# Kernel tuning notes

Measured on AMD Instinct MI355X. Metric: run time of the kernel, lower is better.

## Reference

```python
import jax, jax.numpy as jnp
import numpy as np

N_USER, N_VIDEO, N_PUB, N_TAG = 200000, 100000, 20000, 5000
EMB = 128
HALF = EMB // 2
LAYER_NUM = 3


def setup_inputs() -> dict:
    key = jax.random.key(0)
    ks = jax.random.split(key, 20)
    inp = {
        "user_emb": jax.random.normal(ks[0], (N_USER, EMB), jnp.float32),
        "video_emb": jax.random.normal(ks[1], (N_VIDEO, EMB), jnp.float32),
        "publisher_emb": jax.random.normal(ks[2], (N_PUB, EMB), jnp.float32),
        "tag_emb": jax.random.normal(ks[3], (N_TAG, EMB), jnp.float32),
    }
    # (name, E, n_src, n_dst)
    rels = [
        ("uv", 1500000, N_USER, N_VIDEO),
        ("vu", 1500000, N_VIDEO, N_USER),
        ("up", 800000, N_USER, N_PUB),
        ("pu", 800000, N_PUB, N_USER),
        ("vt", 800000, N_VIDEO, N_TAG),
        ("tv", 800000, N_TAG, N_VIDEO),
        ("pt", 400000, N_PUB, N_TAG),
        ("tp", 400000, N_TAG, N_PUB),
    ]
    for i, (name, E, ns, nd) in enumerate(rels):
        inp[name + "_src"] = jax.random.randint(ks[4 + 2 * i], (E,), 0, ns, jnp.int32)
        inp[name + "_dst"] = jax.random.randint(ks[5 + 2 * i], (E,), 0, nd, jnp.int32)
    return inp


def _seg_mean(feat, src, dst, num_dst):
    # copy_u + mean: gather half-dim src features, segment-mean onto dst.
    msg = feat[src]                                             # [E, HALF]
    s = jax.ops.segment_sum(msg, dst, num_segments=num_dst)     # [num_dst, HALF]
    deg = jax.ops.segment_sum(jnp.ones_like(dst, dtype=feat.dtype), dst,
                              num_segments=num_dst)
    return s / jnp.maximum(deg, 1.0)[:, None]  # zero-in-degree nodes -> 0 (DGL behavior)


def reference(user_emb, video_emb, publisher_emb, tag_emb,
              uv_src, uv_dst, vu_src, vu_dst,
              up_src, up_dst, pu_src, pu_dst,
              vt_src, vt_dst, tv_src, tv_dst,
              pt_src, pt_dst, tp_src, tp_dst):

    def layer(u, v, p, t):
        # user dst: [vu, pu]; video dst: [uv, tv]; publisher dst: [up, tp]; tag dst: [vt, pt]
        vu = _seg_mean(v[:, :HALF], vu_src, vu_dst, N_USER)
        pu = _seg_mean(p[:, :HALF], pu_src, pu_dst, N_USER)
        uv = _seg_mean(u[:, :HALF], uv_src, uv_dst, N_VIDEO)
        tv = _seg_mean(t[:, :HALF], tv_src, tv_dst, N_VIDEO)
        up = _seg_mean(u[:, HALF:], up_src, up_dst, N_PUB)
        tp = _seg_mean(t[:, HALF:], tp_src, tp_dst, N_PUB)
        vt = _seg_mean(v[:, HALF:], vt_src, vt_dst, N_TAG)
        pt = _seg_mean(p[:, HALF:], pt_src, pt_dst, N_TAG)
        return (jnp.concatenate([vu, pu], axis=1),
                jnp.concatenate([uv, tv], axis=1),
                jnp.concatenate([up, tp], axis=1),
                jnp.concatenate([vt, pt], axis=1))

    pu_, pv_, pp_, pt_ = user_emb, video_emb, publisher_emb, tag_emb
    u, v, p, t = user_emb, video_emb, publisher_emb, tag_emb
    for i in range(LAYER_NUM):
        u, v, p, t = layer(u, v, p, t)
        w = 1.0 / (i + 2)
        pu_ = pu_ + u * w
        pv_ = pv_ + v * w
        pp_ = pp_ + p * w
        pt_ = pt_ + t * w
    return (pu_, pv_, pp_, pt_)
```

## Files before the change

kernel.cpp:

```cpp
#include <hip/hip_runtime.h>
#include <hip/hip_bf16.h>
#include <stdint.h>

#define EMB 128
#define CAP 12288

static constexpr int N_USER = 200000, N_VIDEO = 100000, N_PUB = 20000, N_TAG = 5000;
static constexpr int ROW_U = 0, ROW_V = 200000, ROW_P = 300000, ROW_T = 320000;
static constexpr int ROWS = 325000;
static constexpr int TOTAL_E = 7000000;
static constexpr int TOTAL_GROUPS = 650000;
static constexpr int TILE = 4096;

__device__ inline unsigned bf16_rne(float f) {
  unsigned u = __float_as_uint(f);
  return (u + 0x7fffu + ((u >> 16) & 1u)) >> 16;
}
__device__ inline unsigned pack_bf16x2(float lo, float hi) {
  return bf16_rne(lo) | (bf16_rne(hi) << 16);
}

struct SortDesc {
  int tcum[9];
  int bcum[9];
  int gcum[8];
  int E[8];
  int n_dst[8];
  int wshift[8];
  const int* esrc[8];
  const int* edst[8];
};

struct AggrDesc {
  int cum[9];
  int src_base[8];
  int src_col[8];
  int dst_base[8];
  int dst_col[8];
  const float* demb[8];
};

__global__ __launch_bounds__(256) void part_kernel(SortDesc d, uint2* __restrict__ pairs,
                                                   int* __restrict__ cursors) {
  __shared__ int cnt[256];
  __shared__ int lcur[256];
  int blk = blockIdx.x;
  int r = 0;
#pragma unroll
  for (int k = 1; k < 8; ++k) if (blk >= d.tcum[k]) r = k;
  int base = (blk - d.tcum[r]) * TILE;
  int n = min(TILE, d.E[r] - base);
  const int* __restrict__ esrc = d.esrc[r];
  const int* __restrict__ edst = d.edst[r];
  int tid = threadIdx.x;
  int B = d.bcum[r + 1] - d.bcum[r];
  int sh = d.wshift[r];
  int bb = d.bcum[r];
  if (tid < B) cnt[tid] = 0;
  __syncthreads();
  for (int i = tid; i < n; i += 256)
    atomicAdd(&cnt[edst[base + i] >> sh], 1);
  __syncthreads();
  if (tid < B) {
    int c = cnt[tid];
    lcur[tid] = c ? atomicAdd(&cursors[bb + tid], c) : 0;
  }
  __syncthreads();
  for (int i = tid; i < n; i += 256) {
    int dv = edst[base + i];
    int sv = esrc[base + i];
    int b = dv >> sh;
    int pos = atomicAdd(&lcur[b], 1);
    if (pos < CAP) {
      uint2 pr; pr.x = (unsigned)sv; pr.y = (unsigned)dv;
      pairs[(size_t)(bb + b) * CAP + pos] = pr;
    }
  }
}

__global__ __launch_bounds__(256) void bases_kernel(const int* __restrict__ cursors,
                                                    int* __restrict__ bases, int NB) {
  __shared__ int wsums[4];
  int tid = threadIdx.x;
  int L = (NB + 255) / 256;
  int lo = min(tid * L, NB), hi = min(lo + L, NB);
  int s = 0;
  for (int i = lo; i < hi; ++i) s += cursors[i];
  int lane = tid & 63, wv = tid >> 6;
  int v = s;
#pragma unroll
  for (int dd = 1; dd < 64; dd <<= 1) {
    int t = __shfl_up(v, dd);
    if (lane >= dd) v += t;
  }
  if (lane == 63) wsums[wv] = v;
  __syncthreads();
  if (tid == 0) {
    int run = 0;
#pragma unroll
    for (int k = 0; k < 4; ++k) { int t = wsums[k]; wsums[k] = run; run += t; }
  }
  __syncthreads();
  int run = wsums[wv] + (v - s);
  for (int i = lo; i < hi; ++i) { int c = cursors[i]; bases[i] = run; run += c; }
}

__global__ __launch_bounds__(256) void build_kernel(SortDesc d, const uint2* __restrict__ pairs,
                                                    const int* __restrict__ cursors,
                                                    const int* __restrict__ bases,
                                                    int* __restrict__ sorted,
                                                    int* __restrict__ Beg, int* __restrict__ Deg) {
  __shared__ int cnt[1024];
  __shared__ int stage[CAP];
  __shared__ int wsums[4];
  int bucket = blockIdx.x;
  int r = 0;
#pragma unroll
  for (int k = 1; k < 8; ++k) if (bucket >= d.bcum[k]) r = k;
  int bl = bucket - d.bcum[r];
  int sh = d.wshift[r];
  int first = bl << sh;
  int Wa = min(1 << sh, d.n_dst[r] - first);
  int tid = threadIdx.x;
  int n_b = min(cursors[bucket], CAP);
  int gbase = bases[bucket];
  const uint2* __restrict__ bp = pairs + (size_t)bucket * CAP;

  for (int i = tid; i < 1024; i += 256) cnt[i] = 0;
  __syncthreads();
  for (int i = tid; i < n_b; i += 256)
    atomicAdd(&cnt[(int)bp[i].y - first], 1);
  __syncthreads();

  int t4 = tid * 4;
  int c0 = cnt[t4], c1 = cnt[t4 + 1], c2 = cnt[t4 + 2], c3 = cnt[t4 + 3];
  int s = c0 + c1 + c2 + c3;
  int lane = tid & 63, wv = tid >> 6;
  int v = s;
#pragma unroll
  for (int dd = 1; dd < 64; dd <<= 1) {
    int t = __shfl_up(v, dd);
    if (lane >= dd) v += t;
  }
  if (lane == 63) wsums[wv] = v;
  __syncthreads();
  if (tid == 0) {
    int run = 0;
#pragma unroll
    for (int k = 0; k < 4; ++k) { int t = wsums[k]; wsums[k] = run; run += t; }
  }
  __syncthreads();
  int ex = wsums[wv] + (v - s);
  int o0 = ex, o1 = ex + c0, o2 = o1 + c1, o3 = o2 + c2;
  cnt[t4] = o0; cnt[t4 + 1] = o1; cnt[t4 + 2] = o2; cnt[t4 + 3] = o3;
  int g0 = d.gcum[r] + first + t4;
  if (t4 + 0 < Wa) { Beg[g0 + 0] = gbase + o0; Deg[g0 + 0] = c0; }
  if (t4 + 1 < Wa) { Beg[g0 + 1] = gbase + o1; Deg[g0 + 1] = c1; }
  if (t4 + 2 < Wa) { Beg[g0 + 2] = gbase + o2; Deg[g0 + 2] = c2; }
  if (t4 + 3 < Wa) { Beg[g0 + 3] = gbase + o3; Deg[g0 + 3] = c3; }
  __syncthreads();

  for (int i = tid; i < n_b; i += 256) {
    uint2 pr = bp[i];
    int pos = atomicAdd(&cnt[(int)pr.y - first], 1);
    stage[pos] = (int)pr.x;
  }
  __syncthreads();
  for (int i = tid; i < n_b; i += 256)
    sorted[gbase + i] = stage[i];
}

__global__ void convert_kernel(const float* __restrict__ u, const float* __restrict__ v,
                               const float* __restrict__ p, const float* __restrict__ t,
                               uint16_t* __restrict__ feat) {
  int idx = blockIdx.x * blockDim.x + threadIdx.x;
  const int total4 = ROWS * EMB / 4;
  if (idx >= total4) return;
  int flat = idx * 4;
  int row = flat >> 7;
  int col = flat & 127;
  const float* s;
  if (row < ROW_V)      s = u + (size_t)row * EMB + col;
  else if (row < ROW_P) s = v + (size_t)(row - ROW_V) * EMB + col;
  else if (row < ROW_T) s = p + (size_t)(row - ROW_P) * EMB + col;
  else                  s = t + (size_t)(row - ROW_T) * EMB + col;
  float4 f = *(const float4*)s;
  uint2 o;
  o.x = pack_bf16x2(f.x, f.y);
  o.y = pack_bf16x2(f.z, f.w);
  *(uint2*)(feat + flat) = o;
}

#define ACC(q) \
  a0 += __uint_as_float((q).x << 16); a1 += __uint_as_float((q).x & 0xffff0000u); \
  a2 += __uint_as_float((q).y << 16); a3 += __uint_as_float((q).y & 0xffff0000u); \
  a4 += __uint_as_float((q).z << 16); a5 += __uint_as_float((q).z & 0xffff0000u); \
  a6 += __uint_as_float((q).w << 16); a7 += __uint_as_float((q).w & 0xffff0000u);

__global__ __launch_bounds__(256) void aggr_kernel(AggrDesc d, const uint16_t* __restrict__ prev,
                                                   uint16_t* __restrict__ next,
                                                   float* __restrict__ out, float w,
                                                   int layer0, int writeNext,
                                                   const int* __restrict__ sorted,
                                                   const int* __restrict__ Beg,
                                                   const int* __restrict__ Deg) {
  int g = blockIdx.x * 32 + (threadIdx.x >> 3);
  if (g >= TOTAL_GROUPS) return;
  int lane = threadIdx.x & 7;
  int r = 0;
#pragma unroll
  for (int k = 1; k < 8; ++k) if (g >= d.cum[k]) r = k;
  int n = g - d.cum[r];
  int beg = Beg[g], dg = Deg[g];
  float recip = 1.0f / (float)(dg > 0 ? dg : 1);
  const uint16_t* sbase = prev + (size_t)d.src_base[r] * EMB + d.src_col[r] + lane * 8;
  float a0 = 0.f, a1 = 0.f, a2 = 0.f, a3 = 0.f, a4 = 0.f, a5 = 0.f, a6 = 0.f, a7 = 0.f;
  int e = beg, end = beg + dg;
  for (; e + 4 <= end; e += 4) {
    int s0 = sorted[e], s1 = sorted[e + 1], s2 = sorted[e + 2], s3 = sorted[e + 3];
    uint4 q0 = *(const uint4*)(sbase + (size_t)s0 * EMB);
    uint4 q1 = *(const uint4*)(sbase + (size_t)s1 * EMB);
    uint4 q2 = *(const uint4*)(sbase + (size_t)s2 * EMB);
    uint4 q3 = *(const uint4*)(sbase + (size_t)s3 * EMB);
    ACC(q0); ACC(q1); ACC(q2); ACC(q3);
  }
  for (; e < end; ++e) {
    int s0 = sorted[e];
    uint4 q = *(const uint4*)(sbase + (size_t)s0 * EMB);
    ACC(q);
  }
  a0 *= recip; a1 *= recip; a2 *= recip; a3 *= recip;
  a4 *= recip; a5 *= recip; a6 *= recip; a7 *= recip;

  int col = d.dst_col[r] + lane * 8;
  size_t dpos = (size_t)(d.dst_base[r] + n) * EMB + col;
  if (writeNext) {
    uint4 ov;
    ov.x = pack_bf16x2(a0, a1);
    ov.y = pack_bf16x2(a2, a3);
    ov.z = pack_bf16x2(a4, a5);
    ov.w = pack_bf16x2(a6, a7);
    *(uint4*)(next + dpos) = ov;
  }
  float4 v0, v1;
  if (layer0) {
    const float* de = d.demb[r] + (size_t)n * EMB + col;
    v0 = *(const float4*)de;
    v1 = *((const float4*)de + 1);
  } else {
    v0 = *(const float4*)(out + dpos);
    v1 = *((const float4*)(out + dpos) + 1);
  }
  v0.x += w * a0; v0.y += w * a1; v0.z += w * a2; v0.w += w * a3;
  v1.x += w * a4; v1.y += w * a5; v1.z += w * a6; v1.w += w * a7;
  *(float4*)(out + dpos) = v0;
  *((float4*)(out + dpos) + 1) = v1;
}

extern "C" void kernel_launch(void* const* d_in, const int* in_sizes, int n_in,
                              void* d_out, int out_size, void* d_ws, size_t ws_size,
                              hipStream_t stream) {
  const float* emb_u = (const float*)d_in[0];
  const float* emb_v = (const float*)d_in[1];
  const float* emb_p = (const float*)d_in[2];
  const float* emb_t = (const float*)d_in[3];

  struct RelInfo { int si, di, E, n_dst, src_base, src_col, dst_base, dst_col, wshift; };
  const RelInfo rels[8] = {
    {12, 13,  800000, N_TAG,   ROW_V, 64, ROW_T,  0,  5},
    {16, 17,  400000, N_TAG,   ROW_P, 64, ROW_T, 64,  5},
    { 8,  9,  800000, N_PUB,   ROW_U, 64, ROW_P,  0,  7},
    {18, 19,  400000, N_PUB,   ROW_T, 64, ROW_P, 64,  7},
    { 4,  5, 1500000, N_VIDEO, ROW_U,  0, ROW_V,  0,  9},
    {14, 15,  800000, N_VIDEO, ROW_T,  0, ROW_V, 64,  9},
    { 6,  7, 1500000, N_USER,  ROW_V,  0, ROW_U,  0, 10},
    {10, 11,  800000, N_PUB ,  ROW_P,  0, ROW_U, 64, 10},
  };
  const float* dembs[8] = {emb_t, emb_t, emb_p, emb_p, emb_v, emb_v, emb_u, emb_u};

  char* ws = (char*)d_ws;
  size_t cursor = 0;
  auto take = [&](size_t bytes) -> char* {
    char* p = ws + cursor;
    cursor = (cursor + bytes + 255) & ~(size_t)255;
    return p;
  };
  uint16_t* featA = (uint16_t*)take((size_t)ROWS * EMB * 2);
  uint16_t* featB = (uint16_t*)take((size_t)ROWS * EMB * 2);
  int* sorted = (int*)take((size_t)TOTAL_E * 4);
  int* Beg    = (int*)take((size_t)TOTAL_GROUPS * 4);
  int* Deg    = (int*)take((size_t)TOTAL_GROUPS * 4);
  uint2* pairs = (uint2*)d_ws;

  SortDesc sd;
  AggrDesc ad;
  int tacc = 0, bacc = 0, gacc = 0;
  for (int r = 0; r < 8; ++r) {
    int n_dst = (r == 7) ? N_USER : rels[r].n_dst;
    sd.tcum[r] = tacc; tacc += (rels[r].E + TILE - 1) / TILE;
    sd.bcum[r] = bacc; bacc += (n_dst + (1 << rels[r].wshift) - 1) >> rels[r].wshift;
    sd.gcum[r] = gacc;
    sd.E[r] = rels[r].E;
    sd.n_dst[r] = n_dst;
    sd.wshift[r] = rels[r].wshift;
    sd.esrc[r] = (const int*)d_in[rels[r].si];
    sd.edst[r] = (const int*)d_in[rels[r].di];

    ad.cum[r] = gacc;
    ad.src_base[r] = rels[r].src_base;
    ad.src_col[r] = rels[r].src_col;
    ad.dst_base[r] = rels[r].dst_base;
    ad.dst_col[r] = rels[r].dst_col;
    ad.demb[r] = dembs[r];
    gacc += n_dst;
  }
  sd.tcum[8] = tacc;
  sd.bcum[8] = bacc;
  ad.cum[8] = gacc;

  int* cursors = (int*)take((size_t)bacc * 4);
  int* bases   = (int*)take((size_t)bacc * 4);

  hipMemsetAsync(cursors, 0, (size_t)bacc * 4, stream);
  part_kernel<<<tacc, 256, 0, stream>>>(sd, pairs, cursors);
  bases_kernel<<<1, 256, 0, stream>>>(cursors, bases, bacc);
  build_kernel<<<bacc, 256, 0, stream>>>(sd, pairs, cursors, bases, sorted, Beg, Deg);

  convert_kernel<<<(ROWS * EMB / 4 + 255) / 256, 256, 0, stream>>>(emb_u, emb_v, emb_p, emb_t, featA);

  float* out = (float*)d_out;
  uint16_t* prev = featA;
  uint16_t* next = featB;
  const int aggr_blocks = (TOTAL_GROUPS + 31) / 32;
  for (int layer = 0; layer < 3; ++layer) {
    float w = 1.0f / (float)(layer + 2);
    aggr_kernel<<<aggr_blocks, 256, 0, stream>>>(ad, prev, next, out, w,
                                                 layer == 0 ? 1 : 0, layer < 2 ? 1 : 0,
                                                 sorted, Beg, Deg);
    uint16_t* tmp = prev; prev = next; next = tmp;
  }
}
```

Before: 731.4 us.

## Defer output accumulation to last layer and pack edge pairs into 32-bit words

Edge partition pairs are packed into one 32-bit word: the local destination offset goes in the high bits and the source index in the low 18 bits. This halves the scratch traffic between the partition and build kernels. The aggregation kernel no longer does a float32 read-modify-write of the output in the first two layers. The last layer combines the original embedding, the two stored bf16 layer results and the current result with weights 1/2, 1/3 and 1/4, removing two full passes over the fp32 output. The trade-off is that the intermediate layer contributions are summed from bf16 copies rather than fp32 values.

New measurement: 639.5 us. 1.14x faster.

```diff
diff --git a/kernel.cpp b/kernel.cpp
--- a/kernel.cpp
+++ b/kernel.cpp
@@ -40,7 +40,7 @@
   const float* demb[8];
 };
 
-__global__ __launch_bounds__(256) void part_kernel(SortDesc d, uint2* __restrict__ pairs,
+__global__ __launch_bounds__(256) void part_kernel(SortDesc d, unsigned* __restrict__ pairs,
                                                    int* __restrict__ cursors) {
   __shared__ int cnt[256];
   __shared__ int lcur[256];
@@ -55,6 +55,7 @@
   int tid = threadIdx.x;
   int B = d.bcum[r + 1] - d.bcum[r];
   int sh = d.wshift[r];
+  int msk = (1 << sh) - 1;
   int bb = d.bcum[r];
   if (tid < B) cnt[tid] = 0;
   __syncthreads();
@@ -71,10 +72,8 @@
     int sv = esrc[base + i];
     int b = dv >> sh;
     int pos = atomicAdd(&lcur[b], 1);
-    if (pos < CAP) {
-      uint2 pr; pr.x = (unsigned)sv; pr.y = (unsigned)dv;
-      pairs[(size_t)(bb + b) * CAP + pos] = pr;
-    }
+    if (pos < CAP)
+      pairs[(size_t)(bb + b) * CAP + pos] = ((unsigned)(dv & msk) << 18) | (unsigned)sv;
   }
 }
 
@@ -105,7 +104,7 @@
   for (int i = lo; i < hi; ++i) { int c = cursors[i]; bases[i] = run; run += c; }
 }
 
-__global__ __launch_bounds__(256) void build_kernel(SortDesc d, const uint2* __restrict__ pairs,
+__global__ __launch_bounds__(256) void build_kernel(SortDesc d, const unsigned* __restrict__ pairs,
                                                     const int* __restrict__ cursors,
                                                     const int* __restrict__ bases,
                                                     int* __restrict__ sorted,
@@ -124,12 +123,12 @@
   int tid = threadIdx.x;
   int n_b = min(cursors[bucket], CAP);
   int gbase = bases[bucket];
-  const uint2* __restrict__ bp = pairs + (size_t)bucket * CAP;
+  const unsigned* __restrict__ bp = pairs + (size_t)bucket * CAP;
 
   for (int i = tid; i < 1024; i += 256) cnt[i] = 0;
   __syncthreads();
   for (int i = tid; i < n_b; i += 256)
-    atomicAdd(&cnt[(int)bp[i].y - first], 1);
+    atomicAdd(&cnt[bp[i] >> 18], 1);
   __syncthreads();
 
   int t4 = tid * 4;
@@ -161,9 +160,9 @@
   __syncthreads();
 
   for (int i = tid; i < n_b; i += 256) {
-    uint2 pr = bp[i];
-    int pos = atomicAdd(&cnt[(int)pr.y - first], 1);
-    stage[pos] = (int)pr.x;
+    unsigned pr = bp[i];
+    int pos = atomicAdd(&cnt[pr >> 18], 1);
+    stage[pos] = (int)(pr & 0x3FFFFu);
   }
   __syncthreads();
   for (int i = tid; i < n_b; i += 256)
@@ -199,8 +198,7 @@
 
 __global__ __launch_bounds__(256) void aggr_kernel(AggrDesc d, const uint16_t* __restrict__ prev,
                                                    uint16_t* __restrict__ next,
-                                                   float* __restrict__ out, float w,
-                                                   int layer0, int writeNext,
+                                                   float* __restrict__ out, int mode,
                                                    const int* __restrict__ sorted,
                                                    const int* __restrict__ Beg,
                                                    const int* __restrict__ Deg) {
@@ -234,25 +232,31 @@
 
   int col = d.dst_col[r] + lane * 8;
   size_t dpos = (size_t)(d.dst_base[r] + n) * EMB + col;
-  if (writeNext) {
+
+  if (mode == 0) {
     uint4 ov;
     ov.x = pack_bf16x2(a0, a1);
     ov.y = pack_bf16x2(a2, a3);
     ov.z = pack_bf16x2(a4, a5);
     ov.w = pack_bf16x2(a6, a7);
     *(uint4*)(next + dpos) = ov;
-  }
-  float4 v0, v1;
-  if (layer0) {
-    const float* de = d.demb[r] + (size_t)n * EMB + col;
-    v0 = *(const float4*)de;
-    v1 = *((const float4*)de + 1);
-  } else {
-    v0 = *(const float4*)(out + dpos);
-    v1 = *((const float4*)(out + dpos) + 1);
-  }
-  v0.x += w * a0; v0.y += w * a1; v0.z += w * a2; v0.w += w * a3;
-  v1.x += w * a4; v1.y += w * a5; v1.z += w * a6; v1.w += w * a7;
+    return;
+  }
+
+  uint4 q1 = *(const uint4*)(next + dpos);
+  uint4 q2 = *(const uint4*)(prev + dpos);
+  const float* de = d.demb[r] + (size_t)n * EMB + col;
+  float4 v0 = *(const float4*)de;
+  float4 v1 = *((const float4*)de + 1);
+  const float w1 = 0.5f, w2 = 1.0f / 3.0f, w3 = 0.25f;
+  v0.x += w1 * __uint_as_float(q1.x << 16)        + w2 * __uint_as_float(q2.x << 16)        + w3 * a0;
+  v0.y += w1 * __uint_as_float(q1.x & 0xffff0000u) + w2 * __uint_as_float(q2.x & 0xffff0000u) + w3 * a1;
+  v0.z += w1 * __uint_as_float(q1.y << 16)        + w2 * __uint_as_float(q2.y << 16)        + w3 * a2;
+  v0.w += w1 * __uint_as_float(q1.y & 0xffff0000u) + w2 * __uint_as_float(q2.y & 0xffff0000u) + w3 * a3;
+  v1.x += w1 * __uint_as_float(q1.z << 16)        + w2 * __uint_as_float(q2.z << 16)        + w3 * a4;
+  v1.y += w1 * __uint_as_float(q1.z & 0xffff0000u) + w2 * __uint_as_float(q2.z & 0xffff0000u) + w3 * a5;
+  v1.z += w1 * __uint_as_float(q1.w << 16)        + w2 * __uint_as_float(q2.w << 16)        + w3 * a6;
+  v1.w += w1 * __uint_as_float(q1.w & 0xffff0000u) + w2 * __uint_as_float(q2.w & 0xffff0000u) + w3 * a7;
   *(float4*)(out + dpos) = v0;
   *((float4*)(out + dpos) + 1) = v1;
 }
@@ -274,7 +278,7 @@
     { 4,  5, 1500000, N_VIDEO, ROW_U,  0, ROW_V,  0,  9},
     {14, 15,  800000, N_VIDEO, ROW_T,  0, ROW_V, 64,  9},
     { 6,  7, 1500000, N_USER,  ROW_V,  0, ROW_U,  0, 10},
-    {10, 11,  800000, N_PUB ,  ROW_P,  0, ROW_U, 64, 10},
+    {10, 11,  800000, N_USER,  ROW_P,  0, ROW_U, 64, 10},
   };
   const float* dembs[8] = {emb_t, emb_t, emb_p, emb_p, emb_v, emb_v, emb_u, emb_u};
 
@@ -290,13 +294,13 @@
   int* sorted = (int*)take((size_t)TOTAL_E * 4);
   int* Beg    = (int*)take((size_t)TOTAL_GROUPS * 4);
   int* Deg    = (int*)take((size_t)TOTAL_GROUPS * 4);
-  uint2* pairs = (uint2*)d_ws;
+  unsigned* pairs = (unsigned*)d_ws;
 
   SortDesc sd;
   AggrDesc ad;
   int tacc = 0, bacc = 0, gacc = 0;
   for (int r = 0; r < 8; ++r) {
-    int n_dst = (r == 7) ? N_USER : rels[r].n_dst;
+    int n_dst = rels[r].n_dst;
     sd.tcum[r] = tacc; tacc += (rels[r].E + TILE - 1) / TILE;
     sd.bcum[r] = bacc; bacc += (n_dst + (1 << rels[r].wshift) - 1) >> rels[r].wshift;
     sd.gcum[r] = gacc;
@@ -329,14 +333,8 @@
   convert_kernel<<<(ROWS * EMB / 4 + 255) / 256, 256, 0, stream>>>(emb_u, emb_v, emb_p, emb_t, featA);
 
   float* out = (float*)d_out;
-  uint16_t* prev = featA;
-  uint16_t* next = featB;
   const int aggr_blocks = (TOTAL_GROUPS + 31) / 32;
-  for (int layer = 0; layer < 3; ++layer) {
-    float w = 1.0f / (float)(layer + 2);
-    aggr_kernel<<<aggr_blocks, 256, 0, stream>>>(ad, prev, next, out, w,
-                                                 layer == 0 ? 1 : 0, layer < 2 ? 1 : 0,
-                                                 sorted, Beg, Deg);
-    uint16_t* tmp = prev; prev = next; next = tmp;
-  }
-}
+  aggr_kernel<<<aggr_blocks, 256, 0, stream>>>(ad, featA, featB, out, 0, sorted, Beg, Deg);
+  aggr_kernel<<<aggr_blocks, 256, 0, stream>>>(ad, featB, featA, out, 0, sorted, Beg, Deg);
+  aggr_kernel<<<aggr_blocks, 256, 0, stream>>>(ad, featA, featB, out, 1, sorted, Beg, Deg);
+}
```
